# Performance work log

Measured on AMD Instinct MI355X. Metric: run time of the kernel, lower is better.

The kernel has to match this reference:

```python
import jax, jax.numpy as jnp
import numpy as np


def _maxpool(x, k):
    # NCHW max pool with window k, stride k, no padding
    return jax.lax.reduce_window(
        x, -jnp.inf, jax.lax.max,
        window_dimensions=(1, 1, k, k),
        window_strides=(1, 1, k, k),
        padding='VALID')


def setup_inputs() -> dict:
    key = jax.random.key(0)
    k1, k2, k3, k4, k5 = jax.random.split(key, 5)
    return {
        'input_tensor1': jax.random.normal(k1, (8, 128, 56, 56), dtype=jnp.float32),
        'input_tensor2': jax.random.normal(k2, (8, 64, 112, 112), dtype=jnp.float32),
        'input_tensor3': jax.random.normal(k3, (8, 32, 224, 224), dtype=jnp.float32),
        'input_tensor4': jax.random.normal(k4, (8, 16, 448, 448), dtype=jnp.float32),
        'pure_ff': jax.random.normal(k5, (8, 256, 28, 28), dtype=jnp.float32),
    }


def reference(input_tensor1, input_tensor2, input_tensor3, input_tensor4, pure_ff):
    # Original: cat input k times along channels, then maxpool. Pooling is
    # channel-independent, so pool-once-then-tile is mathematically identical
    # (the cat pattern [x,x,...,x] is an exact channel tiling).
    x1 = jnp.tile(_maxpool(input_tensor1, 2), (1, 2, 1, 1))
    x2 = jnp.tile(_maxpool(input_tensor2, 4), (1, 4, 1, 1))
    x3 = jnp.tile(_maxpool(input_tensor3, 8), (1, 8, 1, 1))
    x4 = jnp.tile(_maxpool(input_tensor4, 16), (1, 16, 1, 1))
    return jax.nn.relu(x1 + x2 + x3 + x4 + pure_ff)
```

## Files before the change

### kernel.cpp

```cpp
#include <hip/hip_runtime.h>

#define DEVINL __device__ __forceinline__

DEVINL float fmax4(float4 v) { return fmaxf(fmaxf(v.x, v.y), fmaxf(v.z, v.w)); }
DEVINL float4 max44(float4 a, float4 b) {
    float4 r; r.x = fmaxf(a.x, b.x); r.y = fmaxf(a.y, b.y);
    r.z = fmaxf(a.z, b.z); r.w = fmaxf(a.w, b.w); return r;
}

__global__ __launch_bounds__(256) void fused_pool_relu(
    const float* __restrict__ t1, const float* __restrict__ t2,
    const float* __restrict__ t3, const float* __restrict__ t4,
    const float* __restrict__ ff, float* __restrict__ out)
{
    const int pwq = blockIdx.x;
    const int ph  = blockIdx.y;
    const int b   = blockIdx.z;
    const int tid = threadIdx.x;
    const int pw0 = pwq * 4;

    __shared__ __align__(16) float p1[128 * 4];
    __shared__ __align__(16) float p2[64 * 4];
    __shared__ __align__(16) float p3[32 * 4];
    __shared__ __align__(16) float p4[16 * 4];

    {
        const int g = tid >> 4, l = tid & 15;
        const float* base = t4 + ((size_t)(b * 16 + g) * 448 + ph * 16) * 448
                          + pw0 * 16 + l * 4;
        float4 v[8];
        #pragma unroll
        for (int r = 0; r < 8; ++r) v[r] = *(const float4*)(base + r * 448);
        float4 acc = v[0];
        #pragma unroll
        for (int r = 1; r < 8; ++r) acc = max44(acc, v[r]);
        #pragma unroll
        for (int r = 8; r < 16; ++r) v[r - 8] = *(const float4*)(base + r * 448);
        #pragma unroll
        for (int r = 0; r < 8; ++r) acc = max44(acc, v[r]);
        float m = fmax4(acc);
        m = fmaxf(m, __shfl_xor(m, 1));
        m = fmaxf(m, __shfl_xor(m, 2));
        if ((l & 3) == 0) p4[g * 4 + (l >> 2)] = m;
    }

    {
        const int g = tid >> 3, l = tid & 7;
        const float* base = t3 + ((size_t)(b * 32 + g) * 224 + ph * 8) * 224
                          + pw0 * 8 + l * 4;
        float4 v[8];
        #pragma unroll
        for (int r = 0; r < 8; ++r) v[r] = *(const float4*)(base + r * 224);
        float4 acc = v[0];
        #pragma unroll
        for (int r = 1; r < 8; ++r) acc = max44(acc, v[r]);
        float m = fmax4(acc);
        m = fmaxf(m, __shfl_xor(m, 1));
        if ((l & 1) == 0) p3[g * 4 + (l >> 1)] = m;
    }

    {
        const int g = tid >> 2, l = tid & 3;
        const float* base = t2 + ((size_t)(b * 64 + g) * 112 + ph * 4) * 112
                          + pw0 * 4 + l * 4;
        float4 v[4];
        #pragma unroll
        for (int r = 0; r < 4; ++r) v[r] = *(const float4*)(base + r * 112);
        float4 acc = max44(max44(v[0], v[1]), max44(v[2], v[3]));
        p2[g * 4 + l] = fmax4(acc);
    }

    {
        const int g = tid >> 1, l = tid & 1;
        const float* base = t1 + ((size_t)(b * 128 + g) * 56 + ph * 2) * 56
                          + pw0 * 2 + l * 4;
        float4 v0 = *(const float4*)(base);
        float4 v1 = *(const float4*)(base + 56);
        float4 a = max44(v0, v1);
        p1[g * 4 + l * 2 + 0] = fmaxf(a.x, a.y);
        p1[g * 4 + l * 2 + 1] = fmaxf(a.z, a.w);
    }

    __syncthreads();

    const int c = tid;
    const int o4 = (b * 200704 + c * 784 + ph * 28 + pw0) >> 2;
    const float4 f  = ((const float4*)ff)[o4];
    const float4 a1 = *(const float4*)&p1[(c & 127) * 4];
    const float4 a2 = *(const float4*)&p2[(c & 63) * 4];
    const float4 a3 = *(const float4*)&p3[(c & 31) * 4];
    const float4 a4 = *(const float4*)&p4[(c & 15) * 4];
    float4 o;
    o.x = fmaxf(a1.x + a2.x + a3.x + a4.x + f.x, 0.0f);
    o.y = fmaxf(a1.y + a2.y + a3.y + a4.y + f.y, 0.0f);
    o.z = fmaxf(a1.z + a2.z + a3.z + a4.z + f.z, 0.0f);
    o.w = fmaxf(a1.w + a2.w + a3.w + a4.w + f.w, 0.0f);
    ((float4*)out)[o4] = o;
}

extern "C" void kernel_launch(void* const* d_in, const int* in_sizes, int n_in,
                              void* d_out, int out_size, void* d_ws, size_t ws_size,
                              hipStream_t stream) {
    const float* t1 = (const float*)d_in[0];
    const float* t2 = (const float*)d_in[1];
    const float* t3 = (const float*)d_in[2];
    const float* t4 = (const float*)d_in[3];
    const float* ff = (const float*)d_in[4];
    float* out = (float*)d_out;

    dim3 grid(7, 28, 8);
    fused_pool_relu<<<grid, 256, 0, stream>>>(t1, t2, t3, t4, ff, out);
}
```

Baseline: 229.6 us.

## Split fused pooling into workspace-based pooling pass and combine pass

Replaces the single fused kernel with two kernels. The first pools all four inputs, with each wavefront reading contiguous full rows via coalesced float4 loads, staging partial maxima in shared memory and writing the pooled maps to a workspace. The second reads the pooled maps and pure_ff to produce the relu output. This is meant to fix the poorly coalesced, short-row reads of the original per-output-tile layout, at the cost of an extra launch and a workspace round trip. The original fused kernel is kept as a fallback when the workspace is too small.

```diff
diff --git a/kernel.cpp b/kernel.cpp
--- a/kernel.cpp
+++ b/kernel.cpp
@@ -6,6 +6,157 @@
 DEVINL float4 max44(float4 a, float4 b) {
     float4 r; r.x = fmaxf(a.x, b.x); r.y = fmaxf(a.y, b.y);
     r.z = fmaxf(a.z, b.z); r.w = fmaxf(a.w, b.w); return r;
+}
+
+#define O1 0
+#define O2 802816
+#define O3 1204224
+#define O4 1404928
+#define WS_FLOATS 1505280
+
+#define W_T4 3584
+#define W_T3 10752
+#define W_T2 14336
+#define W_T1 21504
+
+__global__ __launch_bounds__(256, 4) void pool_all(
+    const float* __restrict__ t1, const float* __restrict__ t2,
+    const float* __restrict__ t3, const float* __restrict__ t4,
+    float* __restrict__ ws)
+{
+    __shared__ __align__(16) float scratch[4 * 448];
+    const int tid  = threadIdx.x;
+    const int lane = tid & 63;
+    const int w    = blockIdx.x * 4 + (tid >> 6);
+    float* sm = &scratch[(tid >> 6) * 448];
+
+    if (w < W_T4) {
+        const int ph = w % 28, cb = w / 28;
+        const float* base = t4 + (size_t)cb * 200704 + ph * 7168;
+        float4 acc[7];
+        #pragma unroll
+        for (int k = 0; k < 7; ++k)
+            acc[k] = *(const float4*)(base + (k * 64 + lane) * 4);
+        #pragma unroll
+        for (int g = 1; g < 4; ++g) {
+            float4 v[7];
+            #pragma unroll
+            for (int k = 0; k < 7; ++k)
+                v[k] = *(const float4*)(base + g * 1792 + (k * 64 + lane) * 4);
+            #pragma unroll
+            for (int k = 0; k < 7; ++k) acc[k] = max44(acc[k], v[k]);
+        }
+        #pragma unroll
+        for (int k = 0; k < 7; ++k) {
+            const int p = k * 64 + lane;
+            sm[(p / 112) * 112 + (p % 112)] = fmax4(acc[k]);
+        }
+    } else if (w < W_T3) {
+        const int t = w - W_T4;
+        const int ph = t % 28, cb = t / 28;
+        const float* base = t3 + (size_t)cb * 50176 + ph * 1792;
+        #pragma unroll
+        for (int k = 0; k < 7; ++k) {
+            float4 v = *(const float4*)(base + (k * 64 + lane) * 4);
+            const int p = k * 64 + lane;
+            sm[(p % 56) * 8 + (p / 56)] = fmax4(v);
+        }
+    } else if (w < W_T2) {
+        const int t = w - W_T3;
+        const int phq = t % 7, cb = t / 7;
+        const float* base = t2 + (size_t)cb * 12544 + phq * 1792;
+        #pragma unroll
+        for (int k = 0; k < 7; ++k) {
+            float4 v = *(const float4*)(base + (k * 64 + lane) * 4);
+            const int p = k * 64 + lane;
+            sm[(p % 28) * 16 + (p / 28)] = fmax4(v);
+        }
+    } else {
+        const int t = w - W_T2;
+        const int phq = t % 7, cb = t / 7;
+        const float* base = t1 + (size_t)cb * 3136 + phq * 448;
+        #pragma unroll
+        for (int k = 0; k < 7; ++k) {
+            const float v = base[k * 64 + lane];
+            const int p = k * 64 + lane;
+            sm[(p % 56) * 8 + (p / 56)] = v;
+        }
+    }
+
+    __syncthreads();
+
+    if (w < W_T4) {
+        const int ph = w % 28, cb = w / 28;
+        if (lane < 28) {
+            float4 a = *(const float4*)&sm[0 * 112 + 4 * lane];
+            float4 b = *(const float4*)&sm[1 * 112 + 4 * lane];
+            float4 c = *(const float4*)&sm[2 * 112 + 4 * lane];
+            float4 d = *(const float4*)&sm[3 * 112 + 4 * lane];
+            ws[O4 + cb * 784 + ph * 28 + lane] =
+                fmax4(max44(max44(a, b), max44(c, d)));
+        }
+    } else if (w < W_T3) {
+        const int t = w - W_T4;
+        const int ph = t % 28, cb = t / 28;
+        if (lane < 28) {
+            float4 a = *(const float4*)&sm[16 * lane + 0];
+            float4 b = *(const float4*)&sm[16 * lane + 4];
+            float4 c = *(const float4*)&sm[16 * lane + 8];
+            float4 d = *(const float4*)&sm[16 * lane + 12];
+            ws[O3 + cb * 784 + ph * 28 + lane] =
+                fmax4(max44(max44(a, b), max44(c, d)));
+        }
+    } else if (w < W_T2) {
+        const int t = w - W_T3;
+        const int phq = t % 7, cb = t / 7;
+        if (lane < 56) {
+            #pragma unroll
+            for (int h = 0; h < 2; ++h) {
+                const int o = lane + h * 56;
+                const int pr = o / 28, j = o % 28;
+                float4 v = *(const float4*)&sm[j * 16 + pr * 4];
+                ws[O2 + cb * 784 + phq * 112 + o] = fmax4(v);
+            }
+        }
+    } else {
+        const int t = w - W_T2;
+        const int phq = t % 7, cb = t / 7;
+        if (lane < 56) {
+            #pragma unroll
+            for (int h = 0; h < 2; ++h) {
+                const int o = lane + h * 56;
+                const int pr = o / 28, j = o % 28;
+                float2 a = *(const float2*)&sm[16 * j + 2 * pr];
+                float2 b = *(const float2*)&sm[16 * j + 8 + 2 * pr];
+                ws[O1 + cb * 784 + phq * 112 + o] =
+                    fmaxf(fmaxf(a.x, a.y), fmaxf(b.x, b.y));
+            }
+        }
+    }
+}
+
+__global__ __launch_bounds__(256) void combine(
+    const float* __restrict__ ws, const float* __restrict__ ff,
+    float* __restrict__ out)
+{
+    const int i4 = blockIdx.x * 256 + threadIdx.x;
+    const int pw4 = i4 % 7;
+    const int ph  = (i4 / 7) % 28;
+    const int c   = (i4 / 196) % 256;
+    const int b   = i4 / 50176;
+    const int ppw = ph * 7 + pw4;
+    const float4* W = (const float4*)ws;
+    float4 a1 = W[O1 / 4 + (b * 128 + (c & 127)) * 196 + ppw];
+    float4 a2 = W[O2 / 4 + (b * 64  + (c & 63))  * 196 + ppw];
+    float4 a3 = W[O3 / 4 + (b * 32  + (c & 31))  * 196 + ppw];
+    float4 a4 = W[O4 / 4 + (b * 16  + (c & 15))  * 196 + ppw];
+    float4 f  = ((const float4*)ff)[i4];
+    float4 o;
+    o.x = fmaxf(a1.x + a2.x + a3.x + a4.x + f.x, 0.0f);
+    o.y = fmaxf(a1.y + a2.y + a3.y + a4.y + f.y, 0.0f);
+    o.z = fmaxf(a1.z + a2.z + a3.z + a4.z + f.z, 0.0f);
+    o.w = fmaxf(a1.w + a2.w + a3.w + a4.w + f.w, 0.0f);
+    ((float4*)out)[i4] = o;
 }
 
 __global__ __launch_bounds__(256) void fused_pool_relu(
@@ -13,17 +164,13 @@
     const float* __restrict__ t3, const float* __restrict__ t4,
     const float* __restrict__ ff, float* __restrict__ out)
 {
-    const int pwq = blockIdx.x;
-    const int ph  = blockIdx.y;
-    const int b   = blockIdx.z;
+    const int pwq = blockIdx.x, ph = blockIdx.y, b = blockIdx.z;
     const int tid = threadIdx.x;
     const int pw0 = pwq * 4;
-
     __shared__ __align__(16) float p1[128 * 4];
     __shared__ __align__(16) float p2[64 * 4];
     __shared__ __align__(16) float p3[32 * 4];
     __shared__ __align__(16) float p4[16 * 4];
-
     {
         const int g = tid >> 4, l = tid & 15;
         const float* base = t4 + ((size_t)(b * 16 + g) * 448 + ph * 16) * 448
@@ -43,7 +190,6 @@
         m = fmaxf(m, __shfl_xor(m, 2));
         if ((l & 3) == 0) p4[g * 4 + (l >> 2)] = m;
     }
-
     {
         const int g = tid >> 3, l = tid & 7;
         const float* base = t3 + ((size_t)(b * 32 + g) * 224 + ph * 8) * 224
@@ -58,7 +204,6 @@
         m = fmaxf(m, __shfl_xor(m, 1));
         if ((l & 1) == 0) p3[g * 4 + (l >> 1)] = m;
     }
-
     {
         const int g = tid >> 2, l = tid & 3;
         const float* base = t2 + ((size_t)(b * 64 + g) * 112 + ph * 4) * 112
@@ -66,23 +211,17 @@
         float4 v[4];
         #pragma unroll
         for (int r = 0; r < 4; ++r) v[r] = *(const float4*)(base + r * 112);
-        float4 acc = max44(max44(v[0], v[1]), max44(v[2], v[3]));
-        p2[g * 4 + l] = fmax4(acc);
-    }
-
+        p2[g * 4 + l] = fmax4(max44(max44(v[0], v[1]), max44(v[2], v[3])));
+    }
     {
         const int g = tid >> 1, l = tid & 1;
         const float* base = t1 + ((size_t)(b * 128 + g) * 56 + ph * 2) * 56
                           + pw0 * 2 + l * 4;
-        float4 v0 = *(const float4*)(base);
-        float4 v1 = *(const float4*)(base + 56);
-        float4 a = max44(v0, v1);
+        float4 a = max44(*(const float4*)(base), *(const float4*)(base + 56));
         p1[g * 4 + l * 2 + 0] = fmaxf(a.x, a.y);
         p1[g * 4 + l * 2 + 1] = fmaxf(a.z, a.w);
     }
-
     __syncthreads();
-
     const int c = tid;
     const int o4 = (b * 200704 + c * 784 + ph * 28 + pw0) >> 2;
     const float4 f  = ((const float4*)ff)[o4];
@@ -108,6 +247,12 @@
     const float* ff = (const float*)d_in[4];
     float* out = (float*)d_out;
 
-    dim3 grid(7, 28, 8);
-    fused_pool_relu<<<grid, 256, 0, stream>>>(t1, t2, t3, t4, ff, out);
-}
+    if (ws_size >= (size_t)WS_FLOATS * sizeof(float)) {
+        float* ws = (float*)d_ws;
+        pool_all<<<W_T1 / 4, 256, 0, stream>>>(t1, t2, t3, t4, ws);
+        combine<<<1568, 256, 0, stream>>>(ws, ff, out);
+    } else {
+        dim3 grid(7, 28, 8);
+        fused_pool_relu<<<grid, 256, 0, stream>>>(t1, t2, t3, t4, ff, out);
+    }
+}
```

After: 226.9 us. Within noise of the previous version (-1.2%).
